# Optimization experiments

Measured on AMD Instinct MI355X. Metric: run time of the kernel, lower is better.

## Reference

```python
import jax, jax.numpy as jnp
import numpy as np

B, T, C = 512, 128, 384   # batch, seq (== block_size), embed_dim
H, D = 6, 64              # n_heads, head_size
BLOCK_SIZE = 128


def setup_inputs() -> dict:
    key = jax.random.key(0)
    ks = jax.random.split(key, 6)
    s = C ** -0.5  # init scale, values irrelevant to correctness
    x = jax.random.normal(ks[0], (B, T, C), dtype=jnp.float32)
    Wq = jax.random.normal(ks[1], (H, C, D), dtype=jnp.float32) * s
    Wk = jax.random.normal(ks[2], (H, C, D), dtype=jnp.float32) * s
    Wv = jax.random.normal(ks[3], (H, C, D), dtype=jnp.float32) * s
    Wp = jax.random.normal(ks[4], (H * D, C), dtype=jnp.float32) * s
    bp = jax.random.normal(ks[5], (C,), dtype=jnp.float32) * 0.01
    return {"x": x, "Wq": Wq, "Wk": Wk, "Wv": Wv, "Wp": Wp, "bp": bp}


def reference(x, Wq, Wk, Wv, Wp, bp):
    # Forward of MultiHeadAttentionClass (eval mode: dropout disabled).
    # Heads are vectorized instead of the original Python per-head loop.
    Bx, Tx, Cx = x.shape
    x = x[:, :BLOCK_SIZE, :]                       # truncate to block_size
    t = x.shape[1]
    q = jnp.einsum('btc,hcd->bhtd', x, Wq)         # [B,H,T,D]
    k = jnp.einsum('btc,hcd->bhtd', x, Wk)
    v = jnp.einsum('btc,hcd->bhtd', x, Wv)
    scores = jnp.einsum('bhtd,bhsd->bhts', q, k) * (D ** -0.5)  # [B,H,T,T]
    causal = jnp.tril(jnp.ones((t, t), dtype=bool))
    scores = jnp.where(causal[None, None], scores, -jnp.inf)
    wei = jax.nn.softmax(scores, axis=-1)
    out = jnp.einsum('bhts,bhsd->bhtd', wei, v)    # [B,H,T,D]
    out = out.transpose(0, 2, 1, 3).reshape(x.shape[0], t, H * D)  # concat heads
    out = out @ Wp + bp                            # projection to embed_dim
    return out
```

## Files before the change

### kernel.cpp

```cpp
#include <hip/hip_runtime.h>

#define NB 512
#define NTOK 128
#define NC 384
#define NH 6
#define ND 64

typedef short s16x8 __attribute__((ext_vector_type(8)));
typedef float f32x4 __attribute__((ext_vector_type(4)));

#define MFMA16(a, b, c) __builtin_amdgcn_mfma_f32_16x16x32_bf16((a), (b), (c), 0, 0, 0)

static __device__ __forceinline__ unsigned short f2bf(float f) {
  unsigned int u = __builtin_bit_cast(unsigned int, f);
  u = (u + 0x7FFFu + ((u >> 16) & 1u)) >> 16;
  return (unsigned short)u;
}

static __device__ __forceinline__ uint2 pack4(float a, float b, float c, float d) {
  union { unsigned short h[4]; uint2 u; } t;
  t.h[0] = f2bf(a); t.h[1] = f2bf(b); t.h[2] = f2bf(c); t.h[3] = f2bf(d);
  return t.u;
}

static __device__ __forceinline__ s16x8 cvt8(float4 a, float4 b) {
  union { unsigned short h[8]; s16x8 v; } t;
  t.h[0] = f2bf(a.x); t.h[1] = f2bf(a.y); t.h[2] = f2bf(a.z); t.h[3] = f2bf(a.w);
  t.h[4] = f2bf(b.x); t.h[5] = f2bf(b.y); t.h[6] = f2bf(b.z); t.h[7] = f2bf(b.w);
  return t.v;
}

__global__ __launch_bounds__(256) void convert_weights(
    const float* __restrict__ Wq, const float* __restrict__ Wk,
    const float* __restrict__ Wv, const float* __restrict__ Wp,
    unsigned short* __restrict__ wqkvT, unsigned short* __restrict__ wpT) {
  int idx = blockIdx.x * 256 + threadIdx.x;
  const int NQKV = 3 * NH * ND * NC;
  if (idx < NQKV) {
    int c = idx % NC;
    int d = (idx / NC) % ND;
    int h = (idx / (NC * ND)) % NH;
    int m = idx / (NC * ND * NH);
    const float* W = (m == 0) ? Wq : (m == 1) ? Wk : Wv;
    wqkvT[idx] = f2bf(W[(h * NC + c) * ND + d]);
  } else {
    int j = idx - NQKV;
    int cc = j / NC, r = j % NC;
    wpT[j] = f2bf(Wp[r * NC + cc]);
  }
}

__global__ __launch_bounds__(512, 2) void attn_fused(
    const float* __restrict__ x, const unsigned short* __restrict__ wqkvT,
    unsigned short* __restrict__ O) {
  const int lbid = (blockIdx.x & 7) * 384 + (blockIdx.x >> 3);
  const int b = lbid / NH;
  const int h = lbid % NH;
  const int tid = threadIdx.x;
  const int lane = tid & 63;
  const int l15 = lane & 15;
  const int lg = lane >> 4;
  const int wid = tid >> 6;
  const int r0 = wid * 16;
  const int mw = wid & 3;
  const int nw = wid >> 2;

  __shared__ __align__(16) union {
    unsigned short w[3][64][72];
    unsigned short qs[128][72];
    unsigned short pB[128][136];
  } u;
  __shared__ __align__(16) unsigned short ks[128][72];
  __shared__ __align__(16) unsigned short vts[64][136];

  f32x4 acc[3][2][2];
#pragma unroll
  for (int m = 0; m < 3; ++m)
#pragma unroll
    for (int i = 0; i < 2; ++i)
#pragma unroll
      for (int j = 0; j < 2; ++j) acc[m][i][j] = f32x4{0.f, 0.f, 0.f, 0.f};

  const int wrow = tid >> 3;
  const int wg8 = (tid & 7) * 8;
  const unsigned short* wgp = wqkvT + ((size_t)h * ND + wrow) * NC + wg8;
  const int WM = NH * ND * NC;
  s16x8 wa0 = *(const s16x8*)(wgp);
  s16x8 wa1 = *(const s16x8*)(wgp + WM);
  s16x8 wa2 = *(const s16x8*)(wgp + 2 * WM);

  const float* xr0p = x + ((size_t)b * NTOK + mw * 32 + l15) * NC + lg * 8;
  const float* xr1p = xr0p + 16 * NC;

  for (int kc = 0; kc < 6; ++kc) {
    __syncthreads();
    *(s16x8*)&u.w[0][wrow][wg8] = wa0;
    *(s16x8*)&u.w[1][wrow][wg8] = wa1;
    *(s16x8*)&u.w[2][wrow][wg8] = wa2;
    const float* p0 = xr0p + kc * 64;
    const float* p1 = xr1p + kc * 64;
    float4 f00 = *(const float4*)(p0);      float4 f01 = *(const float4*)(p0 + 4);
    float4 f02 = *(const float4*)(p0 + 32); float4 f03 = *(const float4*)(p0 + 36);
    float4 f10 = *(const float4*)(p1);      float4 f11 = *(const float4*)(p1 + 4);
    float4 f12 = *(const float4*)(p1 + 32); float4 f13 = *(const float4*)(p1 + 36);
    __syncthreads();
    if (kc < 5) {
      wgp += 64;
      wa0 = *(const s16x8*)(wgp);
      wa1 = *(const s16x8*)(wgp + WM);
      wa2 = *(const s16x8*)(wgp + 2 * WM);
    }
    s16x8 a00 = cvt8(f00, f01);
    s16x8 a01 = cvt8(f02, f03);
    s16x8 a10 = cvt8(f10, f11);
    s16x8 a11 = cvt8(f12, f13);
#pragma unroll
    for (int m = 0; m < 3; ++m)
#pragma unroll
      for (int nt2 = 0; nt2 < 2; ++nt2) {
        const int col = nw * 32 + nt2 * 16 + l15;
        s16x8 b0 = *(const s16x8*)&u.w[m][col][lg * 8];
        acc[m][nt2][0] = MFMA16(a00, b0, acc[m][nt2][0]);
        acc[m][nt2][1] = MFMA16(a10, b0, acc[m][nt2][1]);
        s16x8 b1 = *(const s16x8*)&u.w[m][col][32 + lg * 8];
        acc[m][nt2][0] = MFMA16(a01, b1, acc[m][nt2][0]);
        acc[m][nt2][1] = MFMA16(a11, b1, acc[m][nt2][1]);
      }
  }

  __syncthreads();
#pragma unroll
  for (int nt2 = 0; nt2 < 2; ++nt2)
#pragma unroll
    for (int mt = 0; mt < 2; ++mt) {
      const int row = mw * 32 + mt * 16 + 4 * lg;
      const int col = nw * 32 + nt2 * 16 + l15;
#pragma unroll
      for (int r = 0; r < 4; ++r) {
        u.qs[row + r][col] = f2bf(acc[0][nt2][mt][r] * 0.125f);
        ks[row + r][col] = f2bf(acc[1][nt2][mt][r]);
      }
      *(uint2*)&vts[col][row] =
          pack4(acc[2][nt2][mt][0], acc[2][nt2][mt][1],
                acc[2][nt2][mt][2], acc[2][nt2][mt][3]);
    }
  __syncthreads();

  f32x4 sacc[8];
#pragma unroll
  for (int j = 0; j < 8; ++j) sacc[j] = f32x4{0.f, 0.f, 0.f, 0.f};

#pragma unroll
  for (int kd = 0; kd < 2; ++kd) {
    s16x8 bq = *(const s16x8*)&u.qs[r0 + l15][kd * 32 + lg * 8];
#pragma unroll
    for (int nt = 0; nt < 8; ++nt) {
      if (nt <= wid) {
        s16x8 ak = *(const s16x8*)&ks[nt * 16 + l15][kd * 32 + lg * 8];
        sacc[nt] = MFMA16(ak, bq, sacc[nt]);
      }
    }
  }

  const int q = r0 + l15;
  float mx = -1e30f;
#pragma unroll
  for (int nt = 0; nt < 8; ++nt) {
    if (nt <= wid) {
#pragma unroll
      for (int r = 0; r < 4; ++r) {
        int s = nt * 16 + 4 * lg + r;
        float v = (s <= q) ? sacc[nt][r] : -1e30f;
        sacc[nt][r] = v;
        mx = fmaxf(mx, v);
      }
    }
  }
  mx = fmaxf(mx, __shfl_xor(mx, 16, 64));
  mx = fmaxf(mx, __shfl_xor(mx, 32, 64));
  float sm = 0.f;
#pragma unroll
  for (int nt = 0; nt < 8; ++nt) {
    if (nt <= wid) {
#pragma unroll
      for (int r = 0; r < 4; ++r) {
        float e = __expf(sacc[nt][r] - mx);
        sacc[nt][r] = e;
        sm += e;
      }
    }
  }
  sm += __shfl_xor(sm, 16, 64);
  sm += __shfl_xor(sm, 32, 64);
  float inv = 1.f / sm;

  __syncthreads();
#pragma unroll
  for (int nt = 0; nt < 8; ++nt) {
    uint2 pv;
    if (nt <= wid)
      pv = pack4(sacc[nt][0] * inv, sacc[nt][1] * inv, sacc[nt][2] * inv, sacc[nt][3] * inv);
    else { pv.x = 0u; pv.y = 0u; }
    *(uint2*)&u.pB[r0 + l15][nt * 16 + 4 * lg] = pv;
  }
  __syncthreads();

  f32x4 oacc[4];
#pragma unroll
  for (int j = 0; j < 4; ++j) oacc[j] = f32x4{0.f, 0.f, 0.f, 0.f};
#pragma unroll
  for (int kd = 0; kd < 4; ++kd) {
    if (kd * 32 <= r0 + 15) {
      s16x8 bp = *(const s16x8*)&u.pB[r0 + l15][kd * 32 + lg * 8];
#pragma unroll
      for (int dt = 0; dt < 4; ++dt) {
        s16x8 av = *(const s16x8*)&vts[dt * 16 + l15][kd * 32 + lg * 8];
        oacc[dt] = MFMA16(av, bp, oacc[dt]);
      }
    }
  }

  unsigned short* Op = O + ((size_t)(b * NTOK) + r0 + l15) * (NH * ND) + h * ND;
#pragma unroll
  for (int dt = 0; dt < 4; ++dt)
    *(uint2*)&Op[dt * 16 + 4 * lg] =
        pack4(oacc[dt][0], oacc[dt][1], oacc[dt][2], oacc[dt][3]);
}

__global__ __launch_bounds__(256) void proj_gemm(
    const unsigned short* __restrict__ O, const unsigned short* __restrict__ wpT,
    const float* __restrict__ bp, float* __restrict__ out) {
  const int ntile = blockIdx.x >> 9;
  const int mtile = blockIdx.x & 511;
  const int m0 = mtile * 128, n0 = ntile * 128;
  const int tid = threadIdx.x;
  const int lane = tid & 63;
  const int l15 = lane & 15, lg = lane >> 4;
  const int r0 = (tid >> 6) * 32;

  __shared__ __align__(16) unsigned short as_[128][40];
  __shared__ __align__(16) unsigned short bs_[128][40];

  f32x4 acc[2][8];
#pragma unroll
  for (int i = 0; i < 2; ++i)
#pragma unroll
    for (int j = 0; j < 8; ++j) acc[i][j] = f32x4{0.f, 0.f, 0.f, 0.f};

  const int sr = tid >> 2, sc = (tid & 3) * 8;
  const unsigned short* ag = O + (size_t)(m0 + sr) * NC + sc;
  const unsigned short* bg = wpT + (size_t)(n0 + sr) * NC + sc;
  s16x8 ar0 = *(const s16x8*)ag;
  s16x8 ar1 = *(const s16x8*)(ag + (size_t)64 * NC);
  s16x8 br0 = *(const s16x8*)bg;
  s16x8 br1 = *(const s16x8*)(bg + (size_t)64 * NC);

  for (int kc = 0; kc < 12; ++kc) {
    __syncthreads();
    *(s16x8*)&as_[sr][sc] = ar0;  *(s16x8*)&as_[sr + 64][sc] = ar1;
    *(s16x8*)&bs_[sr][sc] = br0;  *(s16x8*)&bs_[sr + 64][sc] = br1;
    __syncthreads();
    if (kc < 11) {
      ag += 32; bg += 32;
      ar0 = *(const s16x8*)ag;  ar1 = *(const s16x8*)(ag + (size_t)64 * NC);
      br0 = *(const s16x8*)bg;  br1 = *(const s16x8*)(bg + (size_t)64 * NC);
    }
    s16x8 a0 = *(const s16x8*)&as_[r0 + l15][lg * 8];
    s16x8 a1 = *(const s16x8*)&as_[r0 + 16 + l15][lg * 8];
#pragma unroll
    for (int nt = 0; nt < 8; ++nt) {
      s16x8 bb = *(const s16x8*)&bs_[nt * 16 + l15][lg * 8];
      acc[0][nt] = MFMA16(a0, bb, acc[0][nt]);
      acc[1][nt] = MFMA16(a1, bb, acc[1][nt]);
    }
  }
#pragma unroll
  for (int mt = 0; mt < 2; ++mt)
#pragma unroll
    for (int nt = 0; nt < 8; ++nt) {
      int trow = m0 + r0 + 16 * mt + 4 * lg;
      int col = n0 + nt * 16 + l15;
      float bias = bp[col];
#pragma unroll
      for (int r = 0; r < 4; ++r)
        out[(size_t)(trow + r) * NC + col] = acc[mt][nt][r] + bias;
    }
}

extern "C" void kernel_launch(void* const* d_in, const int* in_sizes, int n_in,
                              void* d_out, int out_size, void* d_ws, size_t ws_size,
                              hipStream_t stream) {
  const float* x  = (const float*)d_in[0];
  const float* Wq = (const float*)d_in[1];
  const float* Wk = (const float*)d_in[2];
  const float* Wv = (const float*)d_in[3];
  const float* Wp = (const float*)d_in[4];
  const float* bp = (const float*)d_in[5];
  float* out = (float*)d_out;

  char* ws = (char*)d_ws;
  unsigned short* O     = (unsigned short*)(ws);
  unsigned short* wqkvT = (unsigned short*)(ws + 50331648);
  unsigned short* wpT   = (unsigned short*)(ws + 51216384);

  convert_weights<<<2304, 256, 0, stream>>>(Wq, Wk, Wv, Wp, wqkvT, wpT);
  attn_fused<<<NB * NH, 512, 0, stream>>>(x, wqkvT, O);
  proj_gemm<<<3 * 512, 256, 0, stream>>>(O, wpT, bp, out);
}
```

Measured before the change: 436.8 us.

## Pre-convert x to bf16 tiles and stage GEMM operands via direct global-to-LDS loads

Adds a prep kernel that converts x to bf16 in a tiled layout (stored temporarily in the output buffer) and lays out the QKV and projection weights in matching tile images. The attention and projection kernels then use global_load_lds to copy tiles straight into double-buffered LDS, so there is one barrier per k-step and no register staging or in-kernel fp32-to-bf16 conversion. Each head block now reads half-size x, but the extra pass writes and rereads a bf16 copy of x. Reusing d_out as scratch relies on proj_gemm running after attn_fused has consumed it.

```diff
diff --git a/kernel.cpp b/kernel.cpp
--- a/kernel.cpp
+++ b/kernel.cpp
@@ -30,28 +30,58 @@
   return t.v;
 }
 
-__global__ __launch_bounds__(256) void convert_weights(
-    const float* __restrict__ Wq, const float* __restrict__ Wk,
-    const float* __restrict__ Wv, const float* __restrict__ Wp,
-    unsigned short* __restrict__ wqkvT, unsigned short* __restrict__ wpT) {
-  int idx = blockIdx.x * 256 + threadIdx.x;
-  const int NQKV = 3 * NH * ND * NC;
-  if (idx < NQKV) {
-    int c = idx % NC;
-    int d = (idx / NC) % ND;
-    int h = (idx / (NC * ND)) % NH;
-    int m = idx / (NC * ND * NH);
+static __device__ __forceinline__ void g2l16(const void* g, void* l) {
+  __builtin_amdgcn_global_load_lds(
+      (const __attribute__((address_space(1))) unsigned int*)g,
+      (__attribute__((address_space(3))) unsigned int*)l, 16, 0, 0);
+}
+
+#define XGRP 3145728
+#define WGRP 55296
+__global__ __launch_bounds__(256) void prep(
+    const float* __restrict__ x, const float* __restrict__ Wq,
+    const float* __restrict__ Wk, const float* __restrict__ Wv,
+    const float* __restrict__ Wp,
+    unsigned short* __restrict__ xbf, unsigned short* __restrict__ wimg,
+    unsigned short* __restrict__ wpT) {
+  int g = blockIdx.x * 256 + threadIdx.x;
+  if (g < XGRP) {
+    int cg = g & 3;
+    int t = (g >> 2) & 127;
+    int kc = (g >> 9) % 12;
+    int b = g / 6144;
+    const float* src = x + (((size_t)b * NTOK + t) * NC + kc * 32 + cg * 8);
+    float4 f0 = *(const float4*)src;
+    float4 f1 = *(const float4*)(src + 4);
+    *(s16x8*)(xbf + (size_t)g * 8) = cvt8(f0, f1);
+  } else if (g < XGRP + WGRP) {
+    int gw = g - XGRP;
+    int cg = gw & 3;
+    int d = (gw >> 2) & 63;
+    int rem = gw >> 8;
+    int m = rem % 3;
+    int hk = rem / 3;
+    int kc = hk % 12;
+    int h = hk / 12;
     const float* W = (m == 0) ? Wq : (m == 1) ? Wk : Wv;
-    wqkvT[idx] = f2bf(W[(h * NC + c) * ND + d]);
+    const float* s = W + ((size_t)h * NC + kc * 32 + cg * 8) * ND + d;
+    union { unsigned short hh[8]; s16x8 v; } o;
+#pragma unroll
+    for (int j = 0; j < 8; ++j) o.hh[j] = f2bf(s[j * ND]);
+    *(s16x8*)(wimg + (size_t)gw * 8) = o.v;
   } else {
-    int j = idx - NQKV;
-    int cc = j / NC, r = j % NC;
-    wpT[j] = f2bf(Wp[r * NC + cc]);
+    int j = g - XGRP - WGRP;
+    int cc = j / 48;
+    int rb = (j % 48) * 8;
+    union { unsigned short hh[8]; s16x8 v; } o;
+#pragma unroll
+    for (int i = 0; i < 8; ++i) o.hh[i] = f2bf(Wp[(size_t)(rb + i) * NC + cc]);
+    *(s16x8*)(wpT + (size_t)cc * NC + rb) = o.v;
   }
 }
 
 __global__ __launch_bounds__(512, 2) void attn_fused(
-    const float* __restrict__ x, const unsigned short* __restrict__ wqkvT,
+    const unsigned short* __restrict__ xbf, const unsigned short* __restrict__ wimg,
     unsigned short* __restrict__ O) {
   const int lbid = (blockIdx.x & 7) * 384 + (blockIdx.x >> 3);
   const int b = lbid / NH;
@@ -66,11 +96,10 @@
   const int nw = wid >> 2;
 
   __shared__ __align__(16) union {
-    unsigned short w[3][64][72];
-    unsigned short qs[128][72];
+    char dbuf[2][20480];
+    struct { unsigned short qs[128][72]; unsigned short ks[128][72]; } qk;
     unsigned short pB[128][136];
   } u;
-  __shared__ __align__(16) unsigned short ks[128][72];
   __shared__ __align__(16) unsigned short vts[64][136];
 
   f32x4 acc[3][2][2];
@@ -81,50 +110,36 @@
 #pragma unroll
       for (int j = 0; j < 2; ++j) acc[m][i][j] = f32x4{0.f, 0.f, 0.f, 0.f};
 
-  const int wrow = tid >> 3;
-  const int wg8 = (tid & 7) * 8;
-  const unsigned short* wgp = wqkvT + ((size_t)h * ND + wrow) * NC + wg8;
-  const int WM = NH * ND * NC;
-  s16x8 wa0 = *(const s16x8*)(wgp);
-  s16x8 wa1 = *(const s16x8*)(wgp + WM);
-  s16x8 wa2 = *(const s16x8*)(wgp + 2 * WM);
-
-  const float* xr0p = x + ((size_t)b * NTOK + mw * 32 + l15) * NC + lg * 8;
-  const float* xr1p = xr0p + 16 * NC;
-
-  for (int kc = 0; kc < 6; ++kc) {
+  const char* xsrc = (const char*)xbf + (size_t)b * 98304;
+  const char* wsrc = (const char*)wimg + (size_t)h * 147456;
+  const int o16 = tid * 16;
+
+#define STAGE(kc, pg)                                                   \
+  {                                                                     \
+    const char* sx = xsrc + (kc) * 8192;                                \
+    const char* sw = wsrc + (kc) * 12288;                               \
+    char* db = u.dbuf[pg];                                              \
+    g2l16(sx + o16, db + o16);                                          \
+    g2l16(sw + o16, db + 8192 + o16);                                   \
+    if (tid < 256) g2l16(sw + 8192 + o16, db + 16384 + o16);            \
+  }
+
+  STAGE(0, 0);
+  for (int kc = 0; kc < 12; ++kc) {
     __syncthreads();
-    *(s16x8*)&u.w[0][wrow][wg8] = wa0;
-    *(s16x8*)&u.w[1][wrow][wg8] = wa1;
-    *(s16x8*)&u.w[2][wrow][wg8] = wa2;
-    const float* p0 = xr0p + kc * 64;
-    const float* p1 = xr1p + kc * 64;
-    float4 f00 = *(const float4*)(p0);      float4 f01 = *(const float4*)(p0 + 4);
-    float4 f02 = *(const float4*)(p0 + 32); float4 f03 = *(const float4*)(p0 + 36);
-    float4 f10 = *(const float4*)(p1);      float4 f11 = *(const float4*)(p1 + 4);
-    float4 f12 = *(const float4*)(p1 + 32); float4 f13 = *(const float4*)(p1 + 36);
-    __syncthreads();
-    if (kc < 5) {
-      wgp += 64;
-      wa0 = *(const s16x8*)(wgp);
-      wa1 = *(const s16x8*)(wgp + WM);
-      wa2 = *(const s16x8*)(wgp + 2 * WM);
-    }
-    s16x8 a00 = cvt8(f00, f01);
-    s16x8 a01 = cvt8(f02, f03);
-    s16x8 a10 = cvt8(f10, f11);
-    s16x8 a11 = cvt8(f12, f13);
+    if (kc < 11) STAGE(kc + 1, (kc + 1) & 1);
+    const char* cb = u.dbuf[kc & 1];
+    const unsigned short* xs = (const unsigned short*)cb;
+    const unsigned short* wl = (const unsigned short*)(cb + 8192);
+    s16x8 a0 = *(const s16x8*)(xs + (mw * 32 + l15) * 32 + lg * 8);
+    s16x8 a1 = *(const s16x8*)(xs + (mw * 32 + 16 + l15) * 32 + lg * 8);
 #pragma unroll
     for (int m = 0; m < 3; ++m)
 #pragma unroll
       for (int nt2 = 0; nt2 < 2; ++nt2) {
-        const int col = nw * 32 + nt2 * 16 + l15;
-        s16x8 b0 = *(const s16x8*)&u.w[m][col][lg * 8];
-        acc[m][nt2][0] = MFMA16(a00, b0, acc[m][nt2][0]);
-        acc[m][nt2][1] = MFMA16(a10, b0, acc[m][nt2][1]);
-        s16x8 b1 = *(const s16x8*)&u.w[m][col][32 + lg * 8];
-        acc[m][nt2][0] = MFMA16(a01, b1, acc[m][nt2][0]);
-        acc[m][nt2][1] = MFMA16(a11, b1, acc[m][nt2][1]);
+        s16x8 bm = *(const s16x8*)(wl + (m * 64 + nw * 32 + nt2 * 16 + l15) * 32 + lg * 8);
+        acc[m][nt2][0] = MFMA16(a0, bm, acc[m][nt2][0]);
+        acc[m][nt2][1] = MFMA16(a1, bm, acc[m][nt2][1]);
       }
   }
 
@@ -137,8 +152,8 @@
       const int col = nw * 32 + nt2 * 16 + l15;
 #pragma unroll
       for (int r = 0; r < 4; ++r) {
-        u.qs[row + r][col] = f2bf(acc[0][nt2][mt][r] * 0.125f);
-        ks[row + r][col] = f2bf(acc[1][nt2][mt][r]);
+        u.qk.qs[row + r][col] = f2bf(acc[0][nt2][mt][r] * 0.125f);
+        u.qk.ks[row + r][col] = f2bf(acc[1][nt2][mt][r]);
       }
       *(uint2*)&vts[col][row] =
           pack4(acc[2][nt2][mt][0], acc[2][nt2][mt][1],
@@ -152,11 +167,11 @@
 
 #pragma unroll
   for (int kd = 0; kd < 2; ++kd) {
-    s16x8 bq = *(const s16x8*)&u.qs[r0 + l15][kd * 32 + lg * 8];
+    s16x8 bq = *(const s16x8*)&u.qk.qs[r0 + l15][kd * 32 + lg * 8];
 #pragma unroll
     for (int nt = 0; nt < 8; ++nt) {
       if (nt <= wid) {
-        s16x8 ak = *(const s16x8*)&ks[nt * 16 + l15][kd * 32 + lg * 8];
+        s16x8 ak = *(const s16x8*)&u.qk.ks[nt * 16 + l15][kd * 32 + lg * 8];
         sacc[nt] = MFMA16(ak, bq, sacc[nt]);
       }
     }
@@ -227,7 +242,7 @@
         pack4(oacc[dt][0], oacc[dt][1], oacc[dt][2], oacc[dt][3]);
 }
 
-__global__ __launch_bounds__(256) void proj_gemm(
+__global__ __launch_bounds__(256, 2) void proj_gemm(
     const unsigned short* __restrict__ O, const unsigned short* __restrict__ wpT,
     const float* __restrict__ bp, float* __restrict__ out) {
   const int ntile = blockIdx.x >> 9;
@@ -238,8 +253,7 @@
   const int l15 = lane & 15, lg = lane >> 4;
   const int r0 = (tid >> 6) * 32;
 
-  __shared__ __align__(16) unsigned short as_[128][40];
-  __shared__ __align__(16) unsigned short bs_[128][40];
+  __shared__ __align__(16) char db[2][32768];
 
   f32x4 acc[2][8];
 #pragma unroll
@@ -247,31 +261,40 @@
 #pragma unroll
     for (int j = 0; j < 8; ++j) acc[i][j] = f32x4{0.f, 0.f, 0.f, 0.f};
 
-  const int sr = tid >> 2, sc = (tid & 3) * 8;
-  const unsigned short* ag = O + (size_t)(m0 + sr) * NC + sc;
-  const unsigned short* bg = wpT + (size_t)(n0 + sr) * NC + sc;
-  s16x8 ar0 = *(const s16x8*)ag;
-  s16x8 ar1 = *(const s16x8*)(ag + (size_t)64 * NC);
-  s16x8 br0 = *(const s16x8*)bg;
-  s16x8 br1 = *(const s16x8*)(bg + (size_t)64 * NC);
-
-  for (int kc = 0; kc < 12; ++kc) {
+  const char* Ab = (const char*)O + (size_t)m0 * (NC * 2);
+  const char* Bb = (const char*)wpT + (size_t)n0 * (NC * 2);
+
+#define PSTAGE(kc, pg)                                                       \
+  {                                                                          \
+    char* dd = db[pg];                                                       \
+    _Pragma("unroll")                                                        \
+    for (int i = 0; i < 4; ++i) {                                            \
+      int d = i * 4096 + tid * 16;                                           \
+      int kd = d >> 13, row = (d >> 6) & 127, cg = (d >> 4) & 3;             \
+      size_t so = ((size_t)row * NC + (kc) * 64 + kd * 32 + cg * 8) * 2;     \
+      g2l16(Ab + so, dd + d);                                                \
+      g2l16(Bb + so, dd + 16384 + d);                                        \
+    }                                                                        \
+  }
+
+  PSTAGE(0, 0);
+  for (int kc = 0; kc < 6; ++kc) {
     __syncthreads();
-    *(s16x8*)&as_[sr][sc] = ar0;  *(s16x8*)&as_[sr + 64][sc] = ar1;
-    *(s16x8*)&bs_[sr][sc] = br0;  *(s16x8*)&bs_[sr + 64][sc] = br1;
-    __syncthreads();
-    if (kc < 11) {
-      ag += 32; bg += 32;
-      ar0 = *(const s16x8*)ag;  ar1 = *(const s16x8*)(ag + (size_t)64 * NC);
-      br0 = *(const s16x8*)bg;  br1 = *(const s16x8*)(bg + (size_t)64 * NC);
-    }
-    s16x8 a0 = *(const s16x8*)&as_[r0 + l15][lg * 8];
-    s16x8 a1 = *(const s16x8*)&as_[r0 + 16 + l15][lg * 8];
-#pragma unroll
-    for (int nt = 0; nt < 8; ++nt) {
-      s16x8 bb = *(const s16x8*)&bs_[nt * 16 + l15][lg * 8];
-      acc[0][nt] = MFMA16(a0, bb, acc[0][nt]);
-      acc[1][nt] = MFMA16(a1, bb, acc[1][nt]);
+    if (kc < 5) PSTAGE(kc + 1, (kc + 1) & 1);
+    const unsigned short* A = (const unsigned short*)db[kc & 1];
+    const unsigned short* B = (const unsigned short*)(db[kc & 1] + 16384);
+#pragma unroll
+    for (int kd = 0; kd < 2; ++kd) {
+      const unsigned short* Ak = A + kd * 4096;
+      const unsigned short* Bk = B + kd * 4096;
+      s16x8 a0 = *(const s16x8*)(Ak + (r0 + l15) * 32 + lg * 8);
+      s16x8 a1 = *(const s16x8*)(Ak + (r0 + 16 + l15) * 32 + lg * 8);
+#pragma unroll
+      for (int nt = 0; nt < 8; ++nt) {
+        s16x8 bb = *(const s16x8*)(Bk + (nt * 16 + l15) * 32 + lg * 8);
+        acc[0][nt] = MFMA16(a0, bb, acc[0][nt]);
+        acc[1][nt] = MFMA16(a1, bb, acc[1][nt]);
+      }
     }
   }
 #pragma unroll
@@ -299,11 +322,12 @@
   float* out = (float*)d_out;
 
   char* ws = (char*)d_ws;
-  unsigned short* O     = (unsigned short*)(ws);
-  unsigned short* wqkvT = (unsigned short*)(ws + 50331648);
-  unsigned short* wpT   = (unsigned short*)(ws + 51216384);
-
-  convert_weights<<<2304, 256, 0, stream>>>(Wq, Wk, Wv, Wp, wqkvT, wpT);
-  attn_fused<<<NB * NH, 512, 0, stream>>>(x, wqkvT, O);
+  unsigned short* O    = (unsigned short*)(ws);
+  unsigned short* wimg = (unsigned short*)(ws + 50331648);
+  unsigned short* wpT  = (unsigned short*)(ws + 51216384);
+  unsigned short* xbf  = (unsigned short*)d_out;
+
+  prep<<<12576, 256, 0, stream>>>(x, Wq, Wk, Wv, Wp, xbf, wimg, wpT);
+  attn_fused<<<NB * NH, 512, 0, stream>>>(xbf, wimg, O);
   proj_gemm<<<3 * 512, 256, 0, stream>>>(O, wpT, bp, out);
 }
```

New measurement: 362.1 us. -17.1%, faster.
